# Performance work log

Hardware: AMD Instinct MI355X
Metric: run time of the kernel (lower is better)

Reference implementation:

```python
import jax, jax.numpy as jnp
import numpy as np

B, T, D = 8, 1024, 512
H, K, V = 8, 64, 64
DO, DM = 8, 512  # logit_offset feature dim, model_size


def setup_inputs() -> dict:
    key = jax.random.key(0)
    ks = jax.random.split(key, 12)
    s_d = 1.0 / np.sqrt(D)
    s_o = 1.0 / np.sqrt(DO)
    s_hv = 1.0 / np.sqrt(H * V)
    return {
        "query": jax.random.normal(ks[0], (B, T, D), jnp.float32),
        "key": jax.random.normal(ks[1], (B, T, D), jnp.float32),
        "value": jax.random.normal(ks[2], (B, T, D), jnp.float32),
        "logit_offset": jax.random.normal(ks[3], (B, T, T, DO), jnp.float32),
        "mask": jnp.ones((B, T, T), dtype=bool),
        # params (with_bias=False for q/k/v projections)
        "Wq": jax.random.normal(ks[4], (D, H * K), jnp.float32) * s_d,
        "Wk": jax.random.normal(ks[5], (D, H * K), jnp.float32) * s_d,
        "Wv": jax.random.normal(ks[6], (D, H * V), jnp.float32) * s_d,
        "Wo_off": jax.random.normal(ks[7], (DO, H), jnp.float32) * s_o,
        "bo_off": jnp.zeros((H,), jnp.float32),
        "Wout": jax.random.normal(ks[8], (H * V, DM), jnp.float32) * s_hv,
        "bout": jnp.zeros((DM,), jnp.float32),
    }


def reference(query, key, value, logit_offset, mask,
              Wq, Wk, Wv, Wo_off, bo_off, Wout, bout):
    # Projections -> [..., T, H, head_size]
    q = (query @ Wq).reshape(*query.shape[:-1], H, K)
    k = (key @ Wk).reshape(*key.shape[:-1], H, K)
    v = (value @ Wv).reshape(*value.shape[:-1], H, V)

    # Attention logits [..., H, T', T]
    logits = jnp.einsum("...thd,...Thd->...htT", q, k)
    logits = logits / jnp.sqrt(jnp.asarray(K, value.dtype))

    # Head-specific linear map of logit_offset, then move heads axis: [...,T',T,H] -> [...,H,T',T]
    off = logit_offset @ Wo_off + bo_off
    off = jnp.moveaxis(off, -1, -3)
    logits = logits + off

    # mask [..., T', T] -> [..., 1, T', T]
    logits = jnp.where(mask[..., None, :, :], logits, -1e30)

    attn_weights = jax.nn.softmax(logits, axis=-1)  # no dropout (eval)
    attn = jnp.einsum("...htT,...Thd->...thd", attn_weights, v)
    attn = attn.reshape(*query.shape[:-1], H * V)
    return attn @ Wout + bout
```

## Files before the change

kernel.cpp:

```cpp
#include <hip/hip_runtime.h>
#include <stdint.h>
#include <stddef.h>


typedef unsigned short u16;
typedef __attribute__((ext_vector_type(8))) short short8;
typedef __attribute__((ext_vector_type(4))) float f4v;

__device__ __forceinline__ float b2f(u16 u) {
  union { unsigned int i; float f; } v; v.i = ((unsigned int)u) << 16; return v.f;
}
__device__ __forceinline__ u16 f2b(float f) {
  union { unsigned int i; float f; } v; v.f = f;
  unsigned int i = v.i;
  return (u16)((i + 0x7FFFu + ((i >> 16) & 1u)) >> 16);
}
__device__ __forceinline__ short8 cvt8(const float* src) {
  f4v a = *(const f4v*)src;
  f4v b = *(const f4v*)(src + 4);
  short8 s;
  s[0] = (short)f2b(a[0]); s[1] = (short)f2b(a[1]);
  s[2] = (short)f2b(a[2]); s[3] = (short)f2b(a[3]);
  s[4] = (short)f2b(b[0]); s[5] = (short)f2b(b[1]);
  s[6] = (short)f2b(b[2]); s[7] = (short)f2b(b[3]);
  return s;
}

#define GN 512
#define GK 512

template <bool AF32, bool F32OUT>
__device__ __forceinline__ void gemm_body(const void* __restrict__ Av,
                                          const u16* __restrict__ Bt,
                                          void* __restrict__ Cv,
                                          const float* __restrict__ bias) {
  __shared__ __align__(16) u16 As[128 * 40];
  __shared__ __align__(16) u16 Bs[128 * 40];
  const int tid = threadIdx.x;
  const int l = tid & 63;
  const int w = tid >> 6;
  const int wm = w >> 1, wn = w & 1;
  const int ql = l & 15, qq = l >> 4;
  const int m0 = blockIdx.y * 128, n0 = blockIdx.x * 128;

  f4v acc[4][4];
#pragma unroll
  for (int i = 0; i < 4; ++i)
#pragma unroll
    for (int j = 0; j < 4; ++j) acc[i][j] = (f4v)0.0f;

  for (int ko = 0; ko < GK; ko += 32) {
#pragma unroll
    for (int i = 0; i < 2; ++i) {
      int d = i * 256 + tid;
      int row = d >> 2, c = d & 3;
      if (AF32) {
        *(short8*)(As + row * 40 + c * 8) =
            cvt8((const float*)Av + (size_t)(m0 + row) * GK + ko + c * 8);
      } else {
        *(short8*)(As + row * 40 + c * 8) =
            *(const short8*)((const u16*)Av + (size_t)(m0 + row) * GK + ko + c * 8);
      }
      *(short8*)(Bs + row * 40 + c * 8) =
          *(const short8*)(Bt + (size_t)(n0 + row) * GK + ko + c * 8);
    }
    __syncthreads();

    short8 af[4], bf[4];
#pragma unroll
    for (int i = 0; i < 4; ++i) {
      int m = wm * 64 + i * 16 + ql;
      af[i] = *(const short8*)(As + m * 40 + qq * 8);
      int n = wn * 64 + i * 16 + ql;
      bf[i] = *(const short8*)(Bs + n * 40 + qq * 8);
    }
#pragma unroll
    for (int i = 0; i < 4; ++i)
#pragma unroll
      for (int j = 0; j < 4; ++j)
        acc[i][j] = __builtin_amdgcn_mfma_f32_16x16x32_bf16(af[i], bf[j], acc[i][j], 0, 0, 0);
    __syncthreads();
  }

#pragma unroll
  for (int j = 0; j < 4; ++j) {
    int n = n0 + wn * 64 + j * 16 + ql;
    float bv = bias ? bias[n] : 0.0f;
#pragma unroll
    for (int i = 0; i < 4; ++i) {
      int mbase = m0 + wm * 64 + i * 16 + qq * 4;
#pragma unroll
      for (int r = 0; r < 4; ++r) {
        float val = acc[i][j][r] + bv;
        if (F32OUT)
          ((float*)Cv)[(size_t)(mbase + r) * GN + n] = val;
        else
          ((u16*)Cv)[(size_t)(mbase + r) * GN + n] = f2b(val);
      }
    }
  }
}

__global__ __launch_bounds__(256) void gemm_qkv_kernel(
    const float* __restrict__ X0, const float* __restrict__ X1, const float* __restrict__ X2,
    const u16* __restrict__ W0, const u16* __restrict__ W1, const u16* __restrict__ W2,
    u16* __restrict__ Y0, u16* __restrict__ Y1, u16* __restrict__ Y2) {
  int z = blockIdx.z;
  const float* A = (z == 0) ? X0 : (z == 1) ? X1 : X2;
  const u16* Bt = (z == 0) ? W0 : (z == 1) ? W1 : W2;
  u16* C = (z == 0) ? Y0 : (z == 1) ? Y1 : Y2;
  gemm_body<true, false>(A, Bt, C, nullptr);
}

__global__ __launch_bounds__(256) void gemm_out_kernel(
    const u16* __restrict__ A, const u16* __restrict__ Bt,
    float* __restrict__ C, const float* __restrict__ bias) {
  gemm_body<false, true>(A, Bt, C, bias);
}

__global__ void transpose4_kernel(const float* __restrict__ S0, const float* __restrict__ S1,
                                  const float* __restrict__ S2, const float* __restrict__ S3,
                                  u16* __restrict__ D0, u16* __restrict__ D1,
                                  u16* __restrict__ D2, u16* __restrict__ D3) {
  __shared__ u16 tile[32][33];
  int z = blockIdx.z;
  const float* S = (z == 0) ? S0 : (z == 1) ? S1 : (z == 2) ? S2 : S3;
  u16* D = (z == 0) ? D0 : (z == 1) ? D1 : (z == 2) ? D2 : D3;
  int n0 = blockIdx.x * 32, k0 = blockIdx.y * 32;
  int tx = threadIdx.x, ty = threadIdx.y;
  tile[ty][tx] = f2b(S[(k0 + ty) * 512 + n0 + tx]);
  __syncthreads();
  D[(n0 + ty) * 512 + k0 + tx] = tile[tx][ty];
}

__global__ void transpose_v_kernel(const u16* __restrict__ S, u16* __restrict__ D) {
  __shared__ u16 tile[32][33];
  int b = blockIdx.z;
  int t0 = blockIdx.x * 32, c0 = blockIdx.y * 32;
  int tx = threadIdx.x, ty = threadIdx.y;
  tile[ty][tx] = S[((size_t)b * 1024 + t0 + ty) * 512 + c0 + tx];
  __syncthreads();
  D[((size_t)b * 512 + c0 + ty) * 1024 + t0 + tx] = tile[tx][ty];
}

__global__ __launch_bounds__(512) void attn_fused_kernel(
    const u16* __restrict__ Q, const u16* __restrict__ Kp, const u16* __restrict__ VT,
    const float* __restrict__ LO, const float* __restrict__ Wo, const float* __restrict__ bo,
    u16* __restrict__ Oattn) {
  constexpr int T = 1024;
  constexpr int KLD = 520;
  constexpr int VLD = 40;
  constexpr int PLD = 40;
  constexpr int OLD = 33;
  __shared__ __align__(16) u16 Ks[32 * KLD];
  __shared__ __align__(16) u16 Vs[512 * VLD];
  __shared__ __align__(16) u16 Ps[8 * 32 * PLD];
  __shared__ __align__(16) float offs[8 * 32 * OLD];

  const int tid = threadIdx.x;
  const int l = tid & 63;
  const int w = tid >> 6;
  const int ql = l & 15, qq = l >> 4;
  const int qt = blockIdx.x, b = blockIdx.y;

  short8 qf[2][2];
#pragma unroll
  for (int i = 0; i < 2; ++i) {
    const u16* qrow = Q + ((size_t)(b * T + qt * 32 + i * 16 + ql)) * 512 + w * 64;
#pragma unroll
    for (int kk = 0; kk < 2; ++kk)
      qf[i][kk] = *(const short8*)(qrow + kk * 32 + qq * 8);
  }

  float m_r[2][4], l_r[2][4];
  f4v o[2][4];
#pragma unroll
  for (int i = 0; i < 2; ++i)
#pragma unroll
    for (int r = 0; r < 4; ++r) { m_r[i][r] = -1e30f; l_r[i][r] = 0.0f; }
#pragma unroll
  for (int i = 0; i < 2; ++i)
#pragma unroll
    for (int jv = 0; jv < 4; ++jv) o[i][jv] = (f4v)0.0f;

  const float L2E = 1.4426950408889634f;

  const int prow = tid >> 4;
  const int pkey = (tid & 15) * 2;

  for (int t2b = 0; t2b < 32; ++t2b) {
#pragma unroll
    for (int i = 0; i < 4; ++i) {
      int c = i * 512 + tid;
      int row = c >> 6, cc = c & 63;
      *(short8*)(Ks + row * KLD + cc * 8) =
          *(const short8*)(Kp + ((size_t)(b * T + t2b * 32 + row)) * 512 + cc * 8);
    }
#pragma unroll
    for (int i = 0; i < 4; ++i) {
      int c = i * 512 + tid;
      int vd = c >> 2, kc = c & 3;
      *(short8*)(Vs + vd * VLD + kc * 8) =
          *(const short8*)(VT + ((size_t)(b * 512 + vd)) * 1024 + t2b * 32 + kc * 8);
    }
    {
      const float* lop = LO + (((size_t)(b * T + qt * 32 + prow)) * T + t2b * 32 + pkey) * 8;
#pragma unroll
      for (int pp = 0; pp < 2; ++pp) {
        f4v lo0 = *(const f4v*)(lop + pp * 8);
        f4v lo1 = *(const f4v*)(lop + pp * 8 + 4);
#pragma unroll
        for (int hh = 0; hh < 8; ++hh) {
          float off = bo[hh];
          off += lo0[0] * Wo[0 * 8 + hh] + lo0[1] * Wo[1 * 8 + hh] +
                 lo0[2] * Wo[2 * 8 + hh] + lo0[3] * Wo[3 * 8 + hh];
          off += lo1[0] * Wo[4 * 8 + hh] + lo1[1] * Wo[5 * 8 + hh] +
                 lo1[2] * Wo[6 * 8 + hh] + lo1[3] * Wo[7 * 8 + hh];
          offs[hh * (32 * OLD) + prow * OLD + pkey + pp] = off;
        }
      }
    }
    __syncthreads();

    f4v sa[2][2];
#pragma unroll
    for (int i = 0; i < 2; ++i)
#pragma unroll
      for (int jj = 0; jj < 2; ++jj) sa[i][jj] = (f4v)0.0f;
#pragma unroll
    for (int jj = 0; jj < 2; ++jj) {
      int n = jj * 16 + ql;
      short8 kf0 = *(const short8*)(Ks + n * KLD + w * 64 + qq * 8);
      short8 kf1 = *(const short8*)(Ks + n * KLD + w * 64 + 32 + qq * 8);
#pragma unroll
      for (int i = 0; i < 2; ++i) {
        sa[i][jj] = __builtin_amdgcn_mfma_f32_16x16x32_bf16(qf[i][0], kf0, sa[i][jj], 0, 0, 0);
        sa[i][jj] = __builtin_amdgcn_mfma_f32_16x16x32_bf16(qf[i][1], kf1, sa[i][jj], 0, 0, 0);
      }
    }

#pragma unroll
    for (int i = 0; i < 2; ++i) {
#pragma unroll
      for (int r = 0; r < 4; ++r) {
        int row = i * 16 + qq * 4 + r;
        const float* orow = offs + w * (32 * OLD) + row * OLD;
        float z0 = sa[i][0][r] * 0.125f + orow[ql];
        float z1 = sa[i][1][r] * 0.125f + orow[16 + ql];
        float mx = fmaxf(z0, z1);
        mx = fmaxf(mx, __shfl_xor(mx, 1));
        mx = fmaxf(mx, __shfl_xor(mx, 2));
        mx = fmaxf(mx, __shfl_xor(mx, 4));
        mx = fmaxf(mx, __shfl_xor(mx, 8));
        float mn = fmaxf(m_r[i][r], mx);
        float alpha = exp2f((m_r[i][r] - mn) * L2E);
        m_r[i][r] = mn;
        float p0 = exp2f((z0 - mn) * L2E);
        float p1 = exp2f((z1 - mn) * L2E);
        float rs = p0 + p1;
        rs += __shfl_xor(rs, 1);
        rs += __shfl_xor(rs, 2);
        rs += __shfl_xor(rs, 4);
        rs += __shfl_xor(rs, 8);
        l_r[i][r] = l_r[i][r] * alpha + rs;
#pragma unroll
        for (int jv = 0; jv < 4; ++jv) o[i][jv][r] *= alpha;
        Ps[w * (32 * PLD) + row * PLD + ql] = f2b(p0);
        Ps[w * (32 * PLD) + row * PLD + 16 + ql] = f2b(p1);
      }
    }

#pragma unroll
    for (int i = 0; i < 2; ++i) {
      short8 pf = *(const short8*)(Ps + w * (32 * PLD) + (i * 16 + ql) * PLD + qq * 8);
#pragma unroll
      for (int jv = 0; jv < 4; ++jv) {
        short8 vf = *(const short8*)(Vs + (w * 64 + jv * 16 + ql) * VLD + qq * 8);
        o[i][jv] = __builtin_amdgcn_mfma_f32_16x16x32_bf16(pf, vf, o[i][jv], 0, 0, 0);
      }
    }
    __syncthreads();
  }

#pragma unroll
  for (int i = 0; i < 2; ++i)
#pragma unroll
    for (int jv = 0; jv < 4; ++jv)
#pragma unroll
      for (int r = 0; r < 4; ++r) {
        int t = qt * 32 + i * 16 + qq * 4 + r;
        float val = o[i][jv][r] / l_r[i][r];
        Oattn[((size_t)(b * T + t)) * 512 + w * 64 + jv * 16 + ql] = f2b(val);
      }
}

extern "C" void kernel_launch(void* const* d_in, const int* in_sizes, int n_in,
                              void* d_out, int out_size, void* d_ws, size_t ws_size,
                              hipStream_t stream) {
  const float* query = (const float*)d_in[0];
  const float* key   = (const float*)d_in[1];
  const float* value = (const float*)d_in[2];
  const float* LO    = (const float*)d_in[3];
  const float* Wq   = (const float*)d_in[5];
  const float* Wk   = (const float*)d_in[6];
  const float* Wv   = (const float*)d_in[7];
  const float* Wo   = (const float*)d_in[8];
  const float* bo   = (const float*)d_in[9];
  const float* Wout = (const float*)d_in[10];
  const float* bout = (const float*)d_in[11];
  float* out = (float*)d_out;

  u16* ws = (u16*)d_ws;
  u16* WqT   = ws;
  u16* WkT   = WqT + 512 * 512;
  u16* WvT   = WkT + 512 * 512;
  u16* WoutT = WvT + 512 * 512;
  u16* q_ws  = WoutT + 512 * 512;
  u16* k_ws  = q_ws + 8192 * 512;
  u16* v_ws  = k_ws + 8192 * 512;
  u16* vT_ws = v_ws + 8192 * 512;
  u16* a_ws  = vT_ws + 8192 * 512;

  transpose4_kernel<<<dim3(16, 16, 4), dim3(32, 32), 0, stream>>>(
      Wq, Wk, Wv, Wout, WqT, WkT, WvT, WoutT);

  gemm_qkv_kernel<<<dim3(4, 64, 3), dim3(256), 0, stream>>>(
      query, key, value, WqT, WkT, WvT, q_ws, k_ws, v_ws);

  transpose_v_kernel<<<dim3(32, 16, 8), dim3(32, 32), 0, stream>>>(v_ws, vT_ws);

  attn_fused_kernel<<<dim3(32, 8), dim3(512), 0, stream>>>(
      q_ws, k_ws, vT_ws, LO, Wo, bo, a_ws);

  gemm_out_kernel<<<dim3(4, 64, 1), dim3(256), 0, stream>>>(a_ws, WoutT, out, bout);
}
```

Before: 620.0 us.

## Prefetch next K/V/offset tile into registers during attention compute

Global loads for the next key block's K, V^T and logit_offset are issued into registers at the top of each iteration, overlapping their latency with the MFMA and softmax work. The stage is written to LDS after a barrier at the end of the iteration. Wo and bo are also hoisted into registers, and the LDS strides for K and offsets are changed, with offsets now written as float2. This raises register pressure (about 16 vector loads, 64 Wo values and 16 offsets kept live), which may reduce occupancy.

```diff
diff --git a/kernel.cpp b/kernel.cpp
--- a/kernel.cpp
+++ b/kernel.cpp
@@ -148,10 +148,10 @@
     const float* __restrict__ LO, const float* __restrict__ Wo, const float* __restrict__ bo,
     u16* __restrict__ Oattn) {
   constexpr int T = 1024;
-  constexpr int KLD = 520;
+  constexpr int KLD = 552;
   constexpr int VLD = 40;
   constexpr int PLD = 40;
-  constexpr int OLD = 33;
+  constexpr int OLD = 34;
   __shared__ __align__(16) u16 Ks[32 * KLD];
   __shared__ __align__(16) u16 Vs[512 * VLD];
   __shared__ __align__(16) u16 Ps[8 * 32 * PLD];
@@ -163,6 +163,15 @@
   const int ql = l & 15, qq = l >> 4;
   const int qt = blockIdx.x, b = blockIdx.y;
 
+  float wo_r[8][8];
+  float bo_r[8];
+#pragma unroll
+  for (int d = 0; d < 8; ++d)
+#pragma unroll
+    for (int hh = 0; hh < 8; ++hh) wo_r[d][hh] = Wo[d * 8 + hh];
+#pragma unroll
+  for (int hh = 0; hh < 8; ++hh) bo_r[hh] = bo[hh];
+
   short8 qf[2][2];
 #pragma unroll
   for (int i = 0; i < 2; ++i) {
@@ -188,39 +197,76 @@
   const int prow = tid >> 4;
   const int pkey = (tid & 15) * 2;
 
-  for (int t2b = 0; t2b < 32; ++t2b) {
+  short8 kreg[4], vreg[4];
+  f4v loreg[4];
+  float offreg[2][8];
+
+  auto issue_loads = [&](int t2b) {
+    const float* lop = LO + (((size_t)(b * T + qt * 32 + prow)) * T + t2b * 32 + pkey) * 8;
+    loreg[0] = *(const f4v*)(lop);
+    loreg[1] = *(const f4v*)(lop + 4);
+    loreg[2] = *(const f4v*)(lop + 8);
+    loreg[3] = *(const f4v*)(lop + 12);
 #pragma unroll
     for (int i = 0; i < 4; ++i) {
       int c = i * 512 + tid;
       int row = c >> 6, cc = c & 63;
-      *(short8*)(Ks + row * KLD + cc * 8) =
-          *(const short8*)(Kp + ((size_t)(b * T + t2b * 32 + row)) * 512 + cc * 8);
+      kreg[i] = *(const short8*)(Kp + ((size_t)(b * T + t2b * 32 + row)) * 512 + cc * 8);
     }
 #pragma unroll
     for (int i = 0; i < 4; ++i) {
       int c = i * 512 + tid;
       int vd = c >> 2, kc = c & 3;
-      *(short8*)(Vs + vd * VLD + kc * 8) =
-          *(const short8*)(VT + ((size_t)(b * 512 + vd)) * 1024 + t2b * 32 + kc * 8);
-    }
-    {
-      const float* lop = LO + (((size_t)(b * T + qt * 32 + prow)) * T + t2b * 32 + pkey) * 8;
-#pragma unroll
-      for (int pp = 0; pp < 2; ++pp) {
-        f4v lo0 = *(const f4v*)(lop + pp * 8);
-        f4v lo1 = *(const f4v*)(lop + pp * 8 + 4);
-#pragma unroll
-        for (int hh = 0; hh < 8; ++hh) {
-          float off = bo[hh];
-          off += lo0[0] * Wo[0 * 8 + hh] + lo0[1] * Wo[1 * 8 + hh] +
-                 lo0[2] * Wo[2 * 8 + hh] + lo0[3] * Wo[3 * 8 + hh];
-          off += lo1[0] * Wo[4 * 8 + hh] + lo1[1] * Wo[5 * 8 + hh] +
-                 lo1[2] * Wo[6 * 8 + hh] + lo1[3] * Wo[7 * 8 + hh];
-          offs[hh * (32 * OLD) + prow * OLD + pkey + pp] = off;
-        }
-      }
-    }
-    __syncthreads();
+      vreg[i] = *(const short8*)(VT + ((size_t)(b * 512 + vd)) * 1024 + t2b * 32 + kc * 8);
+    }
+  };
+
+  auto compute_dots = [&]() {
+#pragma unroll
+    for (int pp = 0; pp < 2; ++pp) {
+      f4v lo0 = loreg[pp * 2], lo1 = loreg[pp * 2 + 1];
+#pragma unroll
+      for (int hh = 0; hh < 8; ++hh) {
+        float off = bo_r[hh];
+        off += lo0[0] * wo_r[0][hh] + lo0[1] * wo_r[1][hh] +
+               lo0[2] * wo_r[2][hh] + lo0[3] * wo_r[3][hh];
+        off += lo1[0] * wo_r[4][hh] + lo1[1] * wo_r[5][hh] +
+               lo1[2] * wo_r[6][hh] + lo1[3] * wo_r[7][hh];
+        offreg[pp][hh] = off;
+      }
+    }
+  };
+
+  auto write_stage = [&]() {
+#pragma unroll
+    for (int i = 0; i < 4; ++i) {
+      int c = i * 512 + tid;
+      int row = c >> 6, cc = c & 63;
+      *(short8*)(Ks + row * KLD + cc * 8) = kreg[i];
+    }
+#pragma unroll
+    for (int i = 0; i < 4; ++i) {
+      int c = i * 512 + tid;
+      int vd = c >> 2, kc = c & 3;
+      *(short8*)(Vs + vd * VLD + kc * 8) = vreg[i];
+    }
+#pragma unroll
+    for (int hh = 0; hh < 8; ++hh) {
+      float2 val;
+      val.x = offreg[0][hh];
+      val.y = offreg[1][hh];
+      *(float2*)(offs + hh * (32 * OLD) + prow * OLD + pkey) = val;
+    }
+  };
+
+  issue_loads(0);
+  compute_dots();
+  write_stage();
+  __syncthreads();
+
+  for (int t2b = 0; t2b < 32; ++t2b) {
+    const bool pf = (t2b + 1 < 32);
+    if (pf) issue_loads(t2b + 1);
 
     f4v sa[2][2];
 #pragma unroll
@@ -272,14 +318,20 @@
 
 #pragma unroll
     for (int i = 0; i < 2; ++i) {
-      short8 pf = *(const short8*)(Ps + w * (32 * PLD) + (i * 16 + ql) * PLD + qq * 8);
+      short8 pf_ = *(const short8*)(Ps + w * (32 * PLD) + (i * 16 + ql) * PLD + qq * 8);
 #pragma unroll
       for (int jv = 0; jv < 4; ++jv) {
         short8 vf = *(const short8*)(Vs + (w * 64 + jv * 16 + ql) * VLD + qq * 8);
-        o[i][jv] = __builtin_amdgcn_mfma_f32_16x16x32_bf16(pf, vf, o[i][jv], 0, 0, 0);
-      }
-    }
-    __syncthreads();
+        o[i][jv] = __builtin_amdgcn_mfma_f32_16x16x32_bf16(pf_, vf, o[i][jv], 0, 0, 0);
+      }
+    }
+
+    if (pf) {
+      compute_dots();
+      __syncthreads();
+      write_stage();
+      __syncthreads();
+    }
   }
 
 #pragma unroll
```

Result: faster. 563.7 us (-9.1%).
